# Performance work log

Measured on AMD Instinct MI355X. Metric: run time of the kernel, lower is better.

## Reference

```python
import jax, jax.numpy as jnp
import numpy as np

WINDOW = 16  # hardcoded in module __init__

B, S, E, H = 2, 2048, 1024, 16
HD = E // H


def setup_inputs() -> dict:
    key = jax.random.key(0)
    k1, k2, k3, k4, k5, k6 = jax.random.split(key, 6)
    input_embeddings = jax.random.normal(k1, (B, S, E), dtype=jnp.float32)
    token_ids = jax.random.randint(k2, (B, S), 0, 32000, dtype=jnp.int64)
    # nn.MultiheadAttention parameters: packed in_proj (3E, E) + bias, out_proj (E, E) + bias
    in_proj_weight = jax.random.normal(k3, (3 * E, E), dtype=jnp.float32) * 0.02
    in_proj_bias = jax.random.normal(k4, (3 * E,), dtype=jnp.float32) * 0.02
    out_proj_weight = jax.random.normal(k5, (E, E), dtype=jnp.float32) * 0.02
    out_proj_bias = jax.random.normal(k6, (E,), dtype=jnp.float32) * 0.02
    return {
        "input_embeddings": input_embeddings,
        "token_ids": token_ids,
        "in_proj_weight": in_proj_weight,
        "in_proj_bias": in_proj_bias,
        "out_proj_weight": out_proj_weight,
        "out_proj_bias": out_proj_bias,
    }


def _blocked_mask(seq_len: int) -> jnp.ndarray:
    # Module sets mask[i, j] = True for j in [i - WINDOW, i] (17 positions).
    # PyTorch bool attn_mask: True = NOT allowed to attend.
    i = jnp.arange(seq_len)[:, None]
    j = jnp.arange(seq_len)[None, :]
    return (j <= i) & (j >= i - WINDOW)  # [S, S] bool, True = masked out


def reference(input_embeddings, token_ids, in_proj_weight, in_proj_bias,
              out_proj_weight, out_proj_bias):
    x = input_embeddings  # [B, S, E]
    b, s, e = x.shape
    # Packed QKV projection (torch Linear: y = x W^T + b)
    qkv = jnp.einsum('bse,fe->bsf', x, in_proj_weight) + in_proj_bias  # [B, S, 3E]
    q, k, v = jnp.split(qkv, 3, axis=-1)
    # Split heads: [B, H, S, HD]
    q = q.reshape(b, s, H, HD).transpose(0, 2, 1, 3)
    k = k.reshape(b, s, H, HD).transpose(0, 2, 1, 3)
    v = v.reshape(b, s, H, HD).transpose(0, 2, 1, 3)
    scale = 1.0 / jnp.sqrt(jnp.asarray(HD, dtype=x.dtype))
    scores = jnp.einsum('bhqd,bhkd->bhqk', q * scale, k)  # [B, H, S, S]
    blocked = _blocked_mask(s)  # True = masked
    scores = jnp.where(blocked[None, None, :, :], -jnp.inf, scores)
    attn = jax.nn.softmax(scores, axis=-1)
    ctx = jnp.einsum('bhqk,bhkd->bhqd', attn, v)  # [B, H, S, HD]
    ctx = ctx.transpose(0, 2, 1, 3).reshape(b, s, e)
    out = jnp.einsum('bse,fe->bsf', ctx, out_proj_weight) + out_proj_bias
    return out
```

## Files before the change

kernel.cpp:

```cpp
#include <hip/hip_runtime.h>

typedef __attribute__((ext_vector_type(8))) __bf16 bf16x8;
typedef __attribute__((ext_vector_type(4))) float f32x4;
typedef unsigned short u16;
typedef unsigned int u32;

#define MFMA16(a, b, c) __builtin_amdgcn_mfma_f32_16x16x32_bf16((a), (b), (c), 0, 0, 0)

__device__ __forceinline__ u16 f2bf(float f) {
  return (u16)((__float_as_uint(f) + 0x8000u) >> 16);
}

#define BDIM 2
#define SDIM 2048
#define EDIM 1024
#define HDIM 16
#define HD 64
#define MDIM (BDIM * SDIM)

#define SC_C1 0.1803368801111355f
#define SC_C2 4.328085122667252e+01f

#define SW(r) ((((r) & 3) ^ (((r) >> 2) & 3)))

typedef __attribute__((address_space(3))) void lds_void;
typedef __attribute__((address_space(1))) void g_void;

__device__ __forceinline__ void async_lds16(const void* g, void* lds_byte) {
  __builtin_amdgcn_global_load_lds((const g_void*)g, (lds_void*)lds_byte, 16, 0, 0);
}

__global__ __launch_bounds__(256) void cvt_kernel(const float* __restrict__ src,
                                                  u16* __restrict__ dst, int n) {
  int i = (blockIdx.x * 256 + threadIdx.x) * 8;
  if (i >= n) return;
  float4 f0 = *(const float4*)(src + i);
  float4 f1 = *(const float4*)(src + i + 4);
  union { uint4 u; u16 s[8]; } o;
  o.s[0] = f2bf(f0.x); o.s[1] = f2bf(f0.y); o.s[2] = f2bf(f0.z); o.s[3] = f2bf(f0.w);
  o.s[4] = f2bf(f1.x); o.s[5] = f2bf(f1.y); o.s[6] = f2bf(f1.z); o.s[7] = f2bf(f1.w);
  *(uint4*)(dst + i) = o.u;
}

__global__ __launch_bounds__(256) void gemm_qkv_kernel(
    const u16* __restrict__ X, const u16* __restrict__ W,
    const float* __restrict__ bias, u16* __restrict__ qb,
    u16* __restrict__ kb, u16* __restrict__ vtb) {
  __shared__ __align__(16) u16 As[128 * 32];
  __shared__ __align__(16) u16 Bs[128 * 32];
  const int m0 = blockIdx.x * 128, n0 = blockIdx.y * 128;
  const bool isV = (n0 >= 2 * EDIM);
  const int t = threadIdx.x;
  const int l = t & 63;
  const int quad = l >> 4, col = l & 15;
  const int wid = t >> 6;
  const int mh = wid & 1, nh = wid >> 1;
  const int wofs = (t & 192) << 4;
  f32x4 acc[4][4] = {};
  const u16* Ab = X + (size_t)m0 * EDIM;
  const u16* Bb = W + (size_t)n0 * EDIM;
  char* AsB = (char*)As;
  char* BsB = (char*)Bs;

  for (int k0 = 0; k0 < EDIM; k0 += 32) {
    __syncthreads();
#pragma unroll
    for (int p = 0; p < 2; p++) {
      int idx = p * 256 + t;
      int row = idx >> 2;
      int kq = (idx & 3) ^ SW(row);
      async_lds16(Ab + (size_t)row * EDIM + k0 + kq * 8, AsB + p * 4096 + wofs);
      async_lds16(Bb + (size_t)row * EDIM + k0 + kq * 8, BsB + p * 4096 + wofs);
    }
    __syncthreads();
    bf16x8 af[4], bfr[4];
#pragma unroll
    for (int i = 0; i < 4; i++) {
      int ra = 64 * mh + 16 * i + col;
      af[i] = *(const bf16x8*)&As[(ra * 4 + (quad ^ SW(ra))) * 8];
      int rb = 64 * nh + 16 * i + col;
      bfr[i] = *(const bf16x8*)&Bs[(rb * 4 + (quad ^ SW(rb))) * 8];
    }
    if (isV) {
#pragma unroll
      for (int i = 0; i < 4; i++)
#pragma unroll
        for (int j = 0; j < 4; j++)
          acc[i][j] = MFMA16(bfr[i], af[j], acc[i][j]);
    } else {
#pragma unroll
      for (int i = 0; i < 4; i++)
#pragma unroll
        for (int j = 0; j < 4; j++)
          acc[i][j] = MFMA16(af[i], bfr[j], acc[i][j]);
    }
  }

  if (isV) {
#pragma unroll
    for (int i = 0; i < 4; i++)
#pragma unroll
      for (int j = 0; j < 4; j++)
#pragma unroll
        for (int r = 0; r < 4; r++) {
          int n = n0 + 64 * nh + 16 * i + quad * 4 + r;
          int m = m0 + 64 * mh + 16 * j + col;
          float val = acc[i][j][r] + bias[n];
          int e = n & 1023;
          int hh = e >> 6, d = e & 63;
          int bb = m >> 11, s = m & 2047;
          vtb[(((size_t)(bb * HDIM + hh)) * HD + d) * SDIM + s] = f2bf(val);
        }
  } else {
#pragma unroll
    for (int i = 0; i < 4; i++)
#pragma unroll
      for (int j = 0; j < 4; j++)
#pragma unroll
        for (int r = 0; r < 4; r++) {
          int m = m0 + 64 * mh + 16 * i + quad * 4 + r;
          int n = n0 + 64 * nh + 16 * j + col;
          float val = acc[i][j][r] + bias[n];
          int which = n >> 10, e = n & 1023;
          int hh = e >> 6, d = e & 63;
          int bb = m >> 11, s = m & 2047;
          u16* dst = (which == 0) ? qb : kb;
          dst[(((size_t)(bb * HDIM + hh)) * SDIM + s) * HD + d] = f2bf(val);
        }
  }
}

__global__ __launch_bounds__(256) void attn_kernel(
    const u16* __restrict__ qg, const u16* __restrict__ kg,
    const u16* __restrict__ vtg, u16* __restrict__ ctx) {
  __shared__ __align__(16) u16 Ks[64 * 64];
  __shared__ __align__(16) u16 Vs[64 * 64];
  __shared__ __align__(16) u16 Ps[128 * 68];

  const int bh = blockIdx.x;
  const int q0 = blockIdx.y * 128;
  const int t = threadIdx.x;
  const int wid = t >> 6, l = t & 63;
  const int quad = l >> 4, col = l & 15;
  const size_t base = (size_t)bh * SDIM * HD;

  bf16x8 aq[2][2];
#pragma unroll
  for (int sub = 0; sub < 2; sub++) {
    const u16* qp =
        qg + base + (size_t)(q0 + 32 * wid + 16 * sub + col) * HD + quad * 8;
    aq[sub][0] = *(const bf16x8*)(qp);
    aq[sub][1] = *(const bf16x8*)(qp + 32);
  }
  const int qrow0 = q0 + 32 * wid + quad * 4;

  const int srow = t >> 3;
  const int g = (t & 7) ^ (srow & 7);
  const u16* kptr = kg + base + (size_t)srow * HD + g * 8;
  const u16* vptr = vtg + base + (size_t)srow * SDIM + g * 8;
  char* ldsK = (char*)Ks + ((t & 192) << 4);
  char* ldsV = (char*)Vs + ((t & 192) << 4);

  float psum[2][4] = {};
  f32x4 oacc[2][4] = {};

  for (int kt = 0; kt < SDIM / 64; kt++) {
    const int k0 = kt * 64;
    __syncthreads();
    async_lds16(kptr + (size_t)k0 * HD, ldsK);
    async_lds16(kptr + (size_t)(k0 + 32) * HD, ldsK + 4096);
    async_lds16(vptr + k0, ldsV);
    async_lds16(vptr + (size_t)32 * SDIM + k0, ldsV + 4096);
    __syncthreads();

    f32x4 sc[2][4] = {};
#pragma unroll
    for (int half = 0; half < 2; half++)
#pragma unroll
      for (int ct = 0; ct < 4; ct++) {
        int r = 16 * ct + col;
        int phys = (4 * half + quad) ^ (r & 7);
        bf16x8 bfrag = *(const bf16x8*)&Ks[r * 64 + phys * 8];
        sc[0][ct] = MFMA16(aq[0][half], bfrag, sc[0][ct]);
        sc[1][ct] = MFMA16(aq[1][half], bfrag, sc[1][ct]);
      }

    const bool maskt = (k0 <= q0 + 127) && (k0 + 63 >= q0 - 16);
#pragma unroll
    for (int sub = 0; sub < 2; sub++) {
      const int pbase = (32 * wid + 16 * sub + quad * 4) * 68 + col;
      if (maskt) {
#pragma unroll
        for (int ct = 0; ct < 4; ct++)
#pragma unroll
          for (int r = 0; r < 4; r++) {
            int i = qrow0 + 16 * sub + r, j = k0 + 16 * ct + col;
            float arg = sc[sub][ct][r] * SC_C1 - SC_C2;
            arg = (j <= i && j + 16 >= i) ? -1.0e30f : arg;
            float p = __builtin_exp2f(arg);
            psum[sub][r] += p;
            Ps[pbase + r * 68 + 16 * ct] = f2bf(p);
          }
      } else {
#pragma unroll
        for (int ct = 0; ct < 4; ct++)
#pragma unroll
          for (int r = 0; r < 4; r++) {
            float p = __builtin_exp2f(sc[sub][ct][r] * SC_C1 - SC_C2);
            psum[sub][r] += p;
            Ps[pbase + r * 68 + 16 * ct] = f2bf(p);
          }
      }
    }

#pragma unroll
    for (int half = 0; half < 2; half++) {
      bf16x8 pa0 =
          *(const bf16x8*)&Ps[(32 * wid + col) * 68 + half * 32 + quad * 8];
      bf16x8 pa1 =
          *(const bf16x8*)&Ps[(32 * wid + 16 + col) * 68 + half * 32 + quad * 8];
#pragma unroll
      for (int dt = 0; dt < 4; dt++) {
        int vr = 16 * dt + col;
        int phys = (4 * half + quad) ^ (vr & 7);
        bf16x8 vbf = *(const bf16x8*)&Vs[vr * 64 + phys * 8];
        oacc[0][dt] = MFMA16(pa0, vbf, oacc[0][dt]);
        oacc[1][dt] = MFMA16(pa1, vbf, oacc[1][dt]);
      }
    }
  }

#pragma unroll
  for (int off = 1; off < 16; off <<= 1)
#pragma unroll
    for (int sub = 0; sub < 2; sub++)
#pragma unroll
      for (int r = 0; r < 4; r++)
        psum[sub][r] += __shfl_xor(psum[sub][r], off, 64);

  const int b = bh >> 4, h = bh & 15;
#pragma unroll
  for (int sub = 0; sub < 2; sub++) {
    float linv[4];
#pragma unroll
    for (int r = 0; r < 4; r++) linv[r] = 1.0f / psum[sub][r];
#pragma unroll
    for (int dt = 0; dt < 4; dt++)
#pragma unroll
      for (int r = 0; r < 4; r++) {
        int qgl = qrow0 + 16 * sub + r;
        int d = 16 * dt + col;
        ctx[((size_t)(b * SDIM + qgl)) * EDIM + h * HD + d] =
            f2bf(oacc[sub][dt][r] * linv[r]);
      }
  }
}

__global__ __launch_bounds__(256) void gemm_out_kernel(
    const u16* __restrict__ A, const u16* __restrict__ W,
    const float* __restrict__ bias, float* __restrict__ out) {
  __shared__ __align__(16) u16 As[128 * 32];
  __shared__ __align__(16) u16 Bs[128 * 32];
  const int m0 = blockIdx.x * 128, n0 = blockIdx.y * 128;
  const int t = threadIdx.x;
  const int l = t & 63;
  const int quad = l >> 4, col = l & 15;
  const int wid = t >> 6;
  const int mh = wid & 1, nh = wid >> 1;
  const int wofs = (t & 192) << 4;
  f32x4 acc[4][4] = {};
  const u16* Ab = A + (size_t)m0 * EDIM;
  const u16* Bb = W + (size_t)n0 * EDIM;
  char* AsB = (char*)As;
  char* BsB = (char*)Bs;

  for (int k0 = 0; k0 < EDIM; k0 += 32) {
    __syncthreads();
#pragma unroll
    for (int p = 0; p < 2; p++) {
      int idx = p * 256 + t;
      int row = idx >> 2;
      int kq = (idx & 3) ^ SW(row);
      async_lds16(Ab + (size_t)row * EDIM + k0 + kq * 8, AsB + p * 4096 + wofs);
      async_lds16(Bb + (size_t)row * EDIM + k0 + kq * 8, BsB + p * 4096 + wofs);
    }
    __syncthreads();
    bf16x8 af[4], bfr[4];
#pragma unroll
    for (int i = 0; i < 4; i++) {
      int ra = 64 * mh + 16 * i + col;
      af[i] = *(const bf16x8*)&As[(ra * 4 + (quad ^ SW(ra))) * 8];
      int rb = 64 * nh + 16 * i + col;
      bfr[i] = *(const bf16x8*)&Bs[(rb * 4 + (quad ^ SW(rb))) * 8];
    }
#pragma unroll
    for (int i = 0; i < 4; i++)
#pragma unroll
      for (int j = 0; j < 4; j++)
        acc[i][j] = MFMA16(af[i], bfr[j], acc[i][j]);
  }

#pragma unroll
  for (int i = 0; i < 4; i++)
#pragma unroll
    for (int j = 0; j < 4; j++)
#pragma unroll
      for (int r = 0; r < 4; r++) {
        int m = m0 + 64 * mh + 16 * i + quad * 4 + r;
        int n = n0 + 64 * nh + 16 * j + col;
        out[(size_t)m * EDIM + n] = acc[i][j][r] + bias[n];
      }
}

extern "C" void kernel_launch(void* const* d_in, const int* in_sizes, int n_in,
                              void* d_out, int out_size, void* d_ws,
                              size_t ws_size, hipStream_t stream) {
  const float* x = (const float*)d_in[0];
  const float* in_w = (const float*)d_in[2];
  const float* in_b = (const float*)d_in[3];
  const float* out_w = (const float*)d_in[4];
  const float* out_b = (const float*)d_in[5];
  float* out = (float*)d_out;

  char* ws = (char*)d_ws;
  u16* Xb  = (u16*)ws;
  u16* ctx = (u16*)ws;
  u16* qb  = (u16*)(ws + (size_t)( 8 << 20));
  u16* kb  = (u16*)(ws + (size_t)(16 << 20));
  u16* vtb = (u16*)(ws + (size_t)(24 << 20));
  u16* Wib = (u16*)(ws + (size_t)(32 << 20));
  u16* Wob = (u16*)(ws + (size_t)(38 << 20));

  cvt_kernel<<<2048, 256, 0, stream>>>(x, Xb, MDIM * EDIM);
  cvt_kernel<<<1536, 256, 0, stream>>>(in_w, Wib, 3 * EDIM * EDIM);
  cvt_kernel<<<512, 256, 0, stream>>>(out_w, Wob, EDIM * EDIM);

  gemm_qkv_kernel<<<dim3(MDIM / 128, 3 * EDIM / 128), 256, 0, stream>>>(
      Xb, Wib, in_b, qb, kb, vtb);
  attn_kernel<<<dim3(BDIM * HDIM, SDIM / 128), 256, 0, stream>>>(qb, kb, vtb, ctx);
  gemm_out_kernel<<<dim3(MDIM / 128, EDIM / 128), 256, 0, stream>>>(
      ctx, Wob, out_b, out);
}
```

Measured before the change: 225.9 us.

## Double-buffer LDS tiles in GEMM and attention kernels, fuse conversion launches

Converts the QKV GEMM, output GEMM and attention loops to double-buffered LDS staging. The next K/V or A/B tile is issued asynchronously right after a single barrier, so global loads overlap the MFMA work on the current tile, and one barrier per iteration is removed. The three fp32-to-bf16 conversion launches are merged into one kernel that dispatches on index range, cutting launch overhead. LDS usage per block doubles for the staging buffers, which may lower occupancy.

```diff
diff --git a/kernel.cpp b/kernel.cpp
--- a/kernel.cpp
+++ b/kernel.cpp
@@ -30,24 +30,36 @@
   __builtin_amdgcn_global_load_lds((const g_void*)g, (lds_void*)lds_byte, 16, 0, 0);
 }
 
-__global__ __launch_bounds__(256) void cvt_kernel(const float* __restrict__ src,
-                                                  u16* __restrict__ dst, int n) {
+__global__ __launch_bounds__(256) void cvt3_kernel(
+    const float* __restrict__ s0, u16* __restrict__ d0, int n0,
+    const float* __restrict__ s1, u16* __restrict__ d1, int n1,
+    const float* __restrict__ s2, u16* __restrict__ d2, int n2) {
   int i = (blockIdx.x * 256 + threadIdx.x) * 8;
-  if (i >= n) return;
-  float4 f0 = *(const float4*)(src + i);
-  float4 f1 = *(const float4*)(src + i + 4);
-  union { uint4 u; u16 s[8]; } o;
-  o.s[0] = f2bf(f0.x); o.s[1] = f2bf(f0.y); o.s[2] = f2bf(f0.z); o.s[3] = f2bf(f0.w);
-  o.s[4] = f2bf(f1.x); o.s[5] = f2bf(f1.y); o.s[6] = f2bf(f1.z); o.s[7] = f2bf(f1.w);
-  *(uint4*)(dst + i) = o.u;
+  const float* s;
+  u16* d;
+  if (i < n0) {
+    s = s0 + i; d = d0 + i;
+  } else if (i < n0 + n1) {
+    s = s1 + (i - n0); d = d1 + (i - n0);
+  } else if (i < n0 + n1 + n2) {
+    s = s2 + (i - n0 - n1); d = d2 + (i - n0 - n1);
+  } else {
+    return;
+  }
+  float4 f0 = *(const float4*)(s);
+  float4 f1 = *(const float4*)(s + 4);
+  union { uint4 u; u16 h[8]; } o;
+  o.h[0] = f2bf(f0.x); o.h[1] = f2bf(f0.y); o.h[2] = f2bf(f0.z); o.h[3] = f2bf(f0.w);
+  o.h[4] = f2bf(f1.x); o.h[5] = f2bf(f1.y); o.h[6] = f2bf(f1.z); o.h[7] = f2bf(f1.w);
+  *(uint4*)(d) = o.u;
 }
 
 __global__ __launch_bounds__(256) void gemm_qkv_kernel(
     const u16* __restrict__ X, const u16* __restrict__ W,
     const float* __restrict__ bias, u16* __restrict__ qb,
     u16* __restrict__ kb, u16* __restrict__ vtb) {
-  __shared__ __align__(16) u16 As[128 * 32];
-  __shared__ __align__(16) u16 Bs[128 * 32];
+  __shared__ __align__(16) u16 As[2][128 * 32];
+  __shared__ __align__(16) u16 Bs[2][128 * 32];
   const int m0 = blockIdx.x * 128, n0 = blockIdx.y * 128;
   const bool isV = (n0 >= 2 * EDIM);
   const int t = threadIdx.x;
@@ -59,27 +71,32 @@
   f32x4 acc[4][4] = {};
   const u16* Ab = X + (size_t)m0 * EDIM;
   const u16* Bb = W + (size_t)n0 * EDIM;
-  char* AsB = (char*)As;
-  char* BsB = (char*)Bs;
-
-  for (int k0 = 0; k0 < EDIM; k0 += 32) {
-    __syncthreads();
+
+  auto stage = [&](int k0, int buf) {
 #pragma unroll
     for (int p = 0; p < 2; p++) {
       int idx = p * 256 + t;
       int row = idx >> 2;
       int kq = (idx & 3) ^ SW(row);
-      async_lds16(Ab + (size_t)row * EDIM + k0 + kq * 8, AsB + p * 4096 + wofs);
-      async_lds16(Bb + (size_t)row * EDIM + k0 + kq * 8, BsB + p * 4096 + wofs);
-    }
+      async_lds16(Ab + (size_t)row * EDIM + k0 + kq * 8,
+                  (char*)As[buf] + p * 4096 + wofs);
+      async_lds16(Bb + (size_t)row * EDIM + k0 + kq * 8,
+                  (char*)Bs[buf] + p * 4096 + wofs);
+    }
+  };
+
+  stage(0, 0);
+  for (int it = 0; it < EDIM / 32; it++) {
+    const int cur = it & 1;
     __syncthreads();
+    if (it + 1 < EDIM / 32) stage((it + 1) * 32, cur ^ 1);
     bf16x8 af[4], bfr[4];
 #pragma unroll
     for (int i = 0; i < 4; i++) {
       int ra = 64 * mh + 16 * i + col;
-      af[i] = *(const bf16x8*)&As[(ra * 4 + (quad ^ SW(ra))) * 8];
+      af[i] = *(const bf16x8*)&As[cur][(ra * 4 + (quad ^ SW(ra))) * 8];
       int rb = 64 * nh + 16 * i + col;
-      bfr[i] = *(const bf16x8*)&Bs[(rb * 4 + (quad ^ SW(rb))) * 8];
+      bfr[i] = *(const bf16x8*)&Bs[cur][(rb * 4 + (quad ^ SW(rb))) * 8];
     }
     if (isV) {
 #pragma unroll
@@ -133,8 +150,8 @@
 __global__ __launch_bounds__(256) void attn_kernel(
     const u16* __restrict__ qg, const u16* __restrict__ kg,
     const u16* __restrict__ vtg, u16* __restrict__ ctx) {
-  __shared__ __align__(16) u16 Ks[64 * 64];
-  __shared__ __align__(16) u16 Vs[64 * 64];
+  __shared__ __align__(16) u16 Ks[2][64 * 64];
+  __shared__ __align__(16) u16 Vs[2][64 * 64];
   __shared__ __align__(16) u16 Ps[128 * 68];
 
   const int bh = blockIdx.x;
@@ -158,20 +175,27 @@
   const int g = (t & 7) ^ (srow & 7);
   const u16* kptr = kg + base + (size_t)srow * HD + g * 8;
   const u16* vptr = vtg + base + (size_t)srow * SDIM + g * 8;
-  char* ldsK = (char*)Ks + ((t & 192) << 4);
-  char* ldsV = (char*)Vs + ((t & 192) << 4);
-
-  float psum[2][4] = {};
-  f32x4 oacc[2][4] = {};
-
-  for (int kt = 0; kt < SDIM / 64; kt++) {
-    const int k0 = kt * 64;
-    __syncthreads();
+  const int wofs = (t & 192) << 4;
+
+  auto stage = [&](int kt2, int buf) {
+    const int k0 = kt2 * 64;
+    char* ldsK = (char*)Ks[buf] + wofs;
+    char* ldsV = (char*)Vs[buf] + wofs;
     async_lds16(kptr + (size_t)k0 * HD, ldsK);
     async_lds16(kptr + (size_t)(k0 + 32) * HD, ldsK + 4096);
     async_lds16(vptr + k0, ldsV);
     async_lds16(vptr + (size_t)32 * SDIM + k0, ldsV + 4096);
+  };
+
+  float psum[2][4] = {};
+  f32x4 oacc[2][4] = {};
+
+  stage(0, 0);
+  for (int kt = 0; kt < SDIM / 64; kt++) {
+    const int cur = kt & 1;
+    const int k0 = kt * 64;
     __syncthreads();
+    if (kt + 1 < SDIM / 64) stage(kt + 1, cur ^ 1);
 
     f32x4 sc[2][4] = {};
 #pragma unroll
@@ -180,7 +204,7 @@
       for (int ct = 0; ct < 4; ct++) {
         int r = 16 * ct + col;
         int phys = (4 * half + quad) ^ (r & 7);
-        bf16x8 bfrag = *(const bf16x8*)&Ks[r * 64 + phys * 8];
+        bf16x8 bfrag = *(const bf16x8*)&Ks[cur][r * 64 + phys * 8];
         sc[0][ct] = MFMA16(aq[0][half], bfrag, sc[0][ct]);
         sc[1][ct] = MFMA16(aq[1][half], bfrag, sc[1][ct]);
       }
@@ -223,7 +247,7 @@
       for (int dt = 0; dt < 4; dt++) {
         int vr = 16 * dt + col;
         int phys = (4 * half + quad) ^ (vr & 7);
-        bf16x8 vbf = *(const bf16x8*)&Vs[vr * 64 + phys * 8];
+        bf16x8 vbf = *(const bf16x8*)&Vs[cur][vr * 64 + phys * 8];
         oacc[0][dt] = MFMA16(pa0, vbf, oacc[0][dt]);
         oacc[1][dt] = MFMA16(pa1, vbf, oacc[1][dt]);
       }
@@ -259,8 +283,8 @@
 __global__ __launch_bounds__(256) void gemm_out_kernel(
     const u16* __restrict__ A, const u16* __restrict__ W,
     const float* __restrict__ bias, float* __restrict__ out) {
-  __shared__ __align__(16) u16 As[128 * 32];
-  __shared__ __align__(16) u16 Bs[128 * 32];
+  __shared__ __align__(16) u16 As[2][128 * 32];
+  __shared__ __align__(16) u16 Bs[2][128 * 32];
   const int m0 = blockIdx.x * 128, n0 = blockIdx.y * 128;
   const int t = threadIdx.x;
   const int l = t & 63;
@@ -271,27 +295,32 @@
   f32x4 acc[4][4] = {};
   const u16* Ab = A + (size_t)m0 * EDIM;
   const u16* Bb = W + (size_t)n0 * EDIM;
-  char* AsB = (char*)As;
-  char* BsB = (char*)Bs;
-
-  for (int k0 = 0; k0 < EDIM; k0 += 32) {
-    __syncthreads();
+
+  auto stage = [&](int k0, int buf) {
 #pragma unroll
     for (int p = 0; p < 2; p++) {
       int idx = p * 256 + t;
       int row = idx >> 2;
       int kq = (idx & 3) ^ SW(row);
-      async_lds16(Ab + (size_t)row * EDIM + k0 + kq * 8, AsB + p * 4096 + wofs);
-      async_lds16(Bb + (size_t)row * EDIM + k0 + kq * 8, BsB + p * 4096 + wofs);
-    }
+      async_lds16(Ab + (size_t)row * EDIM + k0 + kq * 8,
+                  (char*)As[buf] + p * 4096 + wofs);
+      async_lds16(Bb + (size_t)row * EDIM + k0 + kq * 8,
+                  (char*)Bs[buf] + p * 4096 + wofs);
+    }
+  };
+
+  stage(0, 0);
+  for (int it = 0; it < EDIM / 32; it++) {
+    const int cur = it & 1;
     __syncthreads();
+    if (it + 1 < EDIM / 32) stage((it + 1) * 32, cur ^ 1);
     bf16x8 af[4], bfr[4];
 #pragma unroll
     for (int i = 0; i < 4; i++) {
       int ra = 64 * mh + 16 * i + col;
-      af[i] = *(const bf16x8*)&As[(ra * 4 + (quad ^ SW(ra))) * 8];
+      af[i] = *(const bf16x8*)&As[cur][(ra * 4 + (quad ^ SW(ra))) * 8];
       int rb = 64 * nh + 16 * i + col;
-      bfr[i] = *(const bf16x8*)&Bs[(rb * 4 + (quad ^ SW(rb))) * 8];
+      bfr[i] = *(const bf16x8*)&Bs[cur][(rb * 4 + (quad ^ SW(rb))) * 8];
     }
 #pragma unroll
     for (int i = 0; i < 4; i++)
@@ -331,9 +360,11 @@
   u16* Wib = (u16*)(ws + (size_t)(32 << 20));
   u16* Wob = (u16*)(ws + (size_t)(38 << 20));
 
-  cvt_kernel<<<2048, 256, 0, stream>>>(x, Xb, MDIM * EDIM);
-  cvt_kernel<<<1536, 256, 0, stream>>>(in_w, Wib, 3 * EDIM * EDIM);
-  cvt_kernel<<<512, 256, 0, stream>>>(out_w, Wob, EDIM * EDIM);
+  const int nX = MDIM * EDIM;
+  const int nWi = 3 * EDIM * EDIM;
+  const int nWo = EDIM * EDIM;
+  cvt3_kernel<<<(nX + nWi + nWo) / 8 / 256, 256, 0, stream>>>(
+      x, Xb, nX, in_w, Wib, nWi, out_w, Wob, nWo);
 
   gemm_qkv_kernel<<<dim3(MDIM / 128, 3 * EDIM / 128), 256, 0, stream>>>(
       Xb, Wib, in_b, qb, kb, vtb);
```

Result: slower. 236.8 us (+4.8%).

## Split attention over key range into two partitions and merge conversions

Applied to the files above, without the earlier changes.

Splits the attention key loop into two independent halves (split-K) across a new grid dimension. Unnormalized partial outputs go out in bf16 and row sums in fp32, and a new combine kernel adds the halves and normalizes. The aim is to double attention grid parallelism from 512 blocks, which may underfill the GPU. The three fp32-to-bf16 conversion launches are also fused into one kernel. This adds extra global traffic and a launch for the combine step, plus a second bf16 rounding of the partial outputs.

```diff
diff --git a/kernel.cpp b/kernel.cpp
--- a/kernel.cpp
+++ b/kernel.cpp
@@ -9,6 +9,9 @@
 
 __device__ __forceinline__ u16 f2bf(float f) {
   return (u16)((__float_as_uint(f) + 0x8000u) >> 16);
+}
+__device__ __forceinline__ float bf2f(u16 h) {
+  return __uint_as_float(((u32)h) << 16);
 }
 
 #define BDIM 2
@@ -17,6 +20,7 @@
 #define HDIM 16
 #define HD 64
 #define MDIM (BDIM * SDIM)
+#define NKK 2
 
 #define SC_C1 0.1803368801111355f
 #define SC_C2 4.328085122667252e+01f
@@ -30,16 +34,28 @@
   __builtin_amdgcn_global_load_lds((const g_void*)g, (lds_void*)lds_byte, 16, 0, 0);
 }
 
-__global__ __launch_bounds__(256) void cvt_kernel(const float* __restrict__ src,
-                                                  u16* __restrict__ dst, int n) {
+__global__ __launch_bounds__(256) void cvt3_kernel(
+    const float* __restrict__ s0, u16* __restrict__ d0, int n0,
+    const float* __restrict__ s1, u16* __restrict__ d1, int n1,
+    const float* __restrict__ s2, u16* __restrict__ d2, int n2) {
   int i = (blockIdx.x * 256 + threadIdx.x) * 8;
-  if (i >= n) return;
-  float4 f0 = *(const float4*)(src + i);
-  float4 f1 = *(const float4*)(src + i + 4);
-  union { uint4 u; u16 s[8]; } o;
-  o.s[0] = f2bf(f0.x); o.s[1] = f2bf(f0.y); o.s[2] = f2bf(f0.z); o.s[3] = f2bf(f0.w);
-  o.s[4] = f2bf(f1.x); o.s[5] = f2bf(f1.y); o.s[6] = f2bf(f1.z); o.s[7] = f2bf(f1.w);
-  *(uint4*)(dst + i) = o.u;
+  const float* s;
+  u16* d;
+  if (i < n0) {
+    s = s0 + i; d = d0 + i;
+  } else if (i < n0 + n1) {
+    s = s1 + (i - n0); d = d1 + (i - n0);
+  } else if (i < n0 + n1 + n2) {
+    s = s2 + (i - n0 - n1); d = d2 + (i - n0 - n1);
+  } else {
+    return;
+  }
+  float4 f0 = *(const float4*)(s);
+  float4 f1 = *(const float4*)(s + 4);
+  union { uint4 u; u16 h[8]; } o;
+  o.h[0] = f2bf(f0.x); o.h[1] = f2bf(f0.y); o.h[2] = f2bf(f0.z); o.h[3] = f2bf(f0.w);
+  o.h[4] = f2bf(f1.x); o.h[5] = f2bf(f1.y); o.h[6] = f2bf(f1.z); o.h[7] = f2bf(f1.w);
+  *(uint4*)(d) = o.u;
 }
 
 __global__ __launch_bounds__(256) void gemm_qkv_kernel(
@@ -132,13 +148,15 @@
 
 __global__ __launch_bounds__(256) void attn_kernel(
     const u16* __restrict__ qg, const u16* __restrict__ kg,
-    const u16* __restrict__ vtg, u16* __restrict__ ctx) {
+    const u16* __restrict__ vtg, u16* __restrict__ opart,
+    float* __restrict__ lpart) {
   __shared__ __align__(16) u16 Ks[64 * 64];
   __shared__ __align__(16) u16 Vs[64 * 64];
   __shared__ __align__(16) u16 Ps[128 * 68];
 
   const int bh = blockIdx.x;
   const int q0 = blockIdx.y * 128;
+  const int kk = blockIdx.z;
   const int t = threadIdx.x;
   const int wid = t >> 6, l = t & 63;
   const int quad = l >> 4, col = l & 15;
@@ -164,7 +182,7 @@
   float psum[2][4] = {};
   f32x4 oacc[2][4] = {};
 
-  for (int kt = 0; kt < SDIM / 64; kt++) {
+  for (int kt = kk * (SDIM / 64 / NKK); kt < (kk + 1) * (SDIM / 64 / NKK); kt++) {
     const int k0 = kt * 64;
     __syncthreads();
     async_lds16(kptr + (size_t)k0 * HD, ldsK);
@@ -238,22 +256,44 @@
       for (int r = 0; r < 4; r++)
         psum[sub][r] += __shfl_xor(psum[sub][r], off, 64);
 
-  const int b = bh >> 4, h = bh & 15;
-#pragma unroll
-  for (int sub = 0; sub < 2; sub++) {
-    float linv[4];
-#pragma unroll
-    for (int r = 0; r < 4; r++) linv[r] = 1.0f / psum[sub][r];
+  u16* op = opart + ((size_t)(kk * BDIM * HDIM) + bh) * SDIM * HD;
+#pragma unroll
+  for (int sub = 0; sub < 2; sub++)
 #pragma unroll
     for (int dt = 0; dt < 4; dt++)
 #pragma unroll
       for (int r = 0; r < 4; r++) {
         int qgl = qrow0 + 16 * sub + r;
-        int d = 16 * dt + col;
-        ctx[((size_t)(b * SDIM + qgl)) * EDIM + h * HD + d] =
-            f2bf(oacc[sub][dt][r] * linv[r]);
-      }
-  }
+        op[(size_t)qgl * HD + 16 * dt + col] = f2bf(oacc[sub][dt][r]);
+      }
+  if (col == 0) {
+    float* lp = lpart + ((size_t)(kk * BDIM * HDIM) + bh) * SDIM;
+#pragma unroll
+    for (int sub = 0; sub < 2; sub++)
+#pragma unroll
+      for (int r = 0; r < 4; r++) lp[qrow0 + 16 * sub + r] = psum[sub][r];
+  }
+}
+
+__global__ __launch_bounds__(256) void combine_kernel(
+    const u16* __restrict__ opart, const float* __restrict__ lpart,
+    u16* __restrict__ ctx) {
+  int idx = blockIdx.x * 256 + threadIdx.x;
+  int d0 = (idx & 7) * 8;
+  int s = (idx >> 3) & (SDIM - 1);
+  int bh = idx >> 14;
+  size_t o_off = ((size_t)bh * SDIM + s) * HD + d0;
+  const size_t kstride = (size_t)(BDIM * HDIM) * SDIM * HD;
+  union { uint4 u; u16 h[8]; } a, b, o;
+  a.u = *(const uint4*)(opart + o_off);
+  b.u = *(const uint4*)(opart + kstride + o_off);
+  float lsum = lpart[(size_t)bh * SDIM + s] +
+               lpart[(size_t)(BDIM * HDIM) * SDIM + (size_t)bh * SDIM + s];
+  float linv = 1.0f / lsum;
+#pragma unroll
+  for (int j = 0; j < 8; j++) o.h[j] = f2bf((bf2f(a.h[j]) + bf2f(b.h[j])) * linv);
+  int bb = bh >> 4, h = bh & 15;
+  *(uint4*)(ctx + ((size_t)(bb * SDIM + s)) * EDIM + h * HD + d0) = o.u;
 }
 
 __global__ __launch_bounds__(256) void gemm_out_kernel(
@@ -323,21 +363,28 @@
   float* out = (float*)d_out;
 
   char* ws = (char*)d_ws;
-  u16* Xb  = (u16*)ws;
-  u16* ctx = (u16*)ws;
-  u16* qb  = (u16*)(ws + (size_t)( 8 << 20));
-  u16* kb  = (u16*)(ws + (size_t)(16 << 20));
-  u16* vtb = (u16*)(ws + (size_t)(24 << 20));
-  u16* Wib = (u16*)(ws + (size_t)(32 << 20));
-  u16* Wob = (u16*)(ws + (size_t)(38 << 20));
-
-  cvt_kernel<<<2048, 256, 0, stream>>>(x, Xb, MDIM * EDIM);
-  cvt_kernel<<<1536, 256, 0, stream>>>(in_w, Wib, 3 * EDIM * EDIM);
-  cvt_kernel<<<512, 256, 0, stream>>>(out_w, Wob, EDIM * EDIM);
+  u16* Xb    = (u16*)ws;
+  u16* ctx   = (u16*)ws;
+  u16* qb    = (u16*)(ws + (size_t)( 8 << 20));
+  u16* kb    = (u16*)(ws + (size_t)(16 << 20));
+  u16* vtb   = (u16*)(ws + (size_t)(24 << 20));
+  u16* Wib   = (u16*)(ws + (size_t)(32 << 20));
+  u16* Wob   = (u16*)(ws + (size_t)(38 << 20));
+  u16* opart = (u16*)(ws + (size_t)(40 << 20));
+  float* lpart = (float*)(ws + (size_t)(56 << 20));
+
+  const int nX = MDIM * EDIM;
+  const int nWi = 3 * EDIM * EDIM;
+  const int nWo = EDIM * EDIM;
+  cvt3_kernel<<<(nX + nWi + nWo) / 8 / 256, 256, 0, stream>>>(
+      x, Xb, nX, in_w, Wib, nWi, out_w, Wob, nWo);
 
   gemm_qkv_kernel<<<dim3(MDIM / 128, 3 * EDIM / 128), 256, 0, stream>>>(
       Xb, Wib, in_b, qb, kb, vtb);
-  attn_kernel<<<dim3(BDIM * HDIM, SDIM / 128), 256, 0, stream>>>(qb, kb, vtb, ctx);
+  attn_kernel<<<dim3(BDIM * HDIM, SDIM / 128, NKK), 256, 0, stream>>>(
+      qb, kb, vtb, opart, lpart);
+  combine_kernel<<<(BDIM * HDIM * SDIM * 8) / 256, 256, 0, stream>>>(
+      opart, lpart, ctx);
   gemm_out_kernel<<<dim3(MDIM / 128, EDIM / 128), 256, 0, stream>>>(
       ctx, Wob, out_b, out);
 }
```

Measured after the change: 232.5 us. 2.9% more time.
